# Kernel optimization log

Hardware: AMD Instinct MI355X
Metric: run time of the kernel (lower is better)

The kernel has to match this reference:

```python
import jax, jax.numpy as jnp
import numpy as np

B, C, N, F_, HID = 512, 3, 128, 256, 128  # batch, channels, nodes(=in_dim), num_f(=seq), gru hidden


def setup_inputs() -> dict:
    key = jax.random.key(0)
    ks = jax.random.split(key, 12)
    s = 0.05
    inp = {
        "X": jax.random.normal(ks[0], (B, N, F_), jnp.float32),
        "H": jax.random.uniform(ks[1], (B, C, N, N), jnp.float32),
        "weight": jnp.full((1, 1), 10.0, jnp.float32),        # nn.init.constant_(weight, 10)
        "soft": jnp.full((C,), 1.0 / C, jnp.float32),          # nn.init.constant_(soft, 1/C)
        "w_ih_f": jax.random.normal(ks[2], (3 * HID, N), jnp.float32) * s,
        "w_hh_f": jax.random.normal(ks[3], (3 * HID, HID), jnp.float32) * s,
        "b_ih_f": jax.random.normal(ks[4], (3 * HID,), jnp.float32) * s,
        "b_hh_f": jax.random.normal(ks[5], (3 * HID,), jnp.float32) * s,
        "w_ih_b": jax.random.normal(ks[6], (3 * HID, N), jnp.float32) * s,
        "w_hh_b": jax.random.normal(ks[7], (3 * HID, HID), jnp.float32) * s,
        "b_ih_b": jax.random.normal(ks[8], (3 * HID,), jnp.float32) * s,
        "b_hh_b": jax.random.normal(ks[9], (3 * HID,), jnp.float32) * s,
        "bn_gamma": jnp.ones((F_,), jnp.float32),
        "bn_beta": jnp.zeros((F_,), jnp.float32),
    }
    return inp


def _gru_dir(xs, w_ih, w_hh, b_ih, b_hh):
    # xs: [T, B, in] -> ys: [T, B, HID]; torch GRU cell equations
    def cell(h, x):
        gi = x @ w_ih.T + b_ih
        gh = h @ w_hh.T + b_hh
        i_r, i_z, i_n = jnp.split(gi, 3, axis=-1)
        h_r, h_z, h_n = jnp.split(gh, 3, axis=-1)
        r = jax.nn.sigmoid(i_r + h_r)
        z = jax.nn.sigmoid(i_z + h_z)
        n = jnp.tanh(i_n + r * h_n)
        h_new = (1.0 - z) * n + z * h
        return h_new, h_new
    h0 = jnp.zeros((xs.shape[1], w_hh.shape[1]), xs.dtype)
    _, ys = jax.lax.scan(cell, h0, xs)
    return ys


def reference(X, H, weight, soft, w_ih_f, w_hh_f, b_ih_f, b_hh_f,
              w_ih_b, w_hh_b, b_ih_b, b_hh_b, bn_gamma, bn_beta):
    n = X.shape[1]
    I = jnp.eye(n, dtype=X.dtype)
    # norm(): zero the diagonal, add identity, symmetric D^-1/2 H D^-1/2 (all C channels at once)
    Hn = H * (1.0 - I) + I                              # [B,C,N,N]
    deg = jnp.sum(Hn, axis=-1)                          # [B,C,N]
    dinv = deg ** -0.5
    Hn = dinv[..., :, None] * Hn * dinv[..., None, :]
    # gcn_conv across all features/channels in one einsum; weight is a 1x1 scalar
    HX = jnp.einsum('bcnm,bmf->bcnf', Hn, X) * weight[0, 0]
    Xc = jnp.sum(jax.nn.leaky_relu(HX, 0.01) * soft[None, :, None, None], axis=1)  # [B,N,F]
    # per1 -> [B, F, N]; GRU batch_first with seq_len=F, input=N
    xs = Xc.transpose(2, 0, 1)                          # [T=F, B, N]
    yf = _gru_dir(xs, w_ih_f, w_hh_f, b_ih_f, b_hh_f)
    yb = _gru_dir(xs[::-1], w_ih_b, w_hh_b, b_ih_b, b_hh_b)[::-1]
    y = jnp.concatenate([yf, yb], axis=-1).transpose(1, 0, 2)  # [B, F, 2*HID]

    # BatchNorm1d(num_f), training-mode batch stats over (batch, length) per channel F
    mean = jnp.mean(y, axis=(0, 2), keepdims=True)
    var = jnp.var(y, axis=(0, 2), keepdims=True)
    y = bn_gamma[None, :, None] * (y - mean) / jnp.sqrt(var + 1e-5) + bn_beta[None, :, None]
    # per2 -> [B, 2*HID, F]
    return y.transpose(0, 2, 1)
```

## Files before the change

kernel.cpp:

```cpp
#include <hip/hip_runtime.h>

typedef short s8v  __attribute__((ext_vector_type(8)));
typedef float f4v  __attribute__((ext_vector_type(4)));

#define B_   512
#define C_   3
#define N_   128
#define F_   256
#define T_   256
#define HID_ 128
#define G3_  384

__device__ __forceinline__ ushort f2bf(float f) {
  union { float f; unsigned u; } v; v.f = f;
  return (ushort)((v.u + 0x7FFFu + ((v.u >> 16) & 1u)) >> 16);
}
__device__ __forceinline__ float bf2f(ushort h) {
  union { unsigned u; float f; } v; v.u = ((unsigned)h) << 16;
  return v.f;
}
__device__ __forceinline__ float rcp_(float x) { return __builtin_amdgcn_rcpf(x); }
__device__ __forceinline__ float sigm(float x) { return rcp_(1.0f + __expf(-x)); }
__device__ __forceinline__ float tanh_(float x) { return 2.0f * rcp_(1.0f + __expf(-2.0f * x)) - 1.0f; }

#define LDS_BARRIER() asm volatile("s_waitcnt lgkmcnt(0)\n\ts_barrier" ::: "memory")

__global__ void k_wcvt(const float* __restrict__ a, const float* __restrict__ b,
                       const float* __restrict__ c, const float* __restrict__ d,
                       ushort* __restrict__ o) {
  int i = blockIdx.x * 256 + threadIdx.x;
  const float* src = (i < 49152) ? a : (i < 98304) ? b : (i < 147456) ? c : d;
  o[i] = f2bf(src[i % 49152]);
}

__global__ void k_dinv(const float* __restrict__ H, float* __restrict__ dinv) {
  const int bc = blockIdx.x;
  const int lane = threadIdx.x & 63, w = threadIdx.x >> 6;
  const float* Hm = H + (size_t)bc * N_ * N_;
  for (int r = w * 32; r < w * 32 + 32; ++r) {
    float a = Hm[(size_t)r * N_ + lane];
    float b = Hm[(size_t)r * N_ + 64 + lane];
    if (lane == r) a = 1.0f;
    if (64 + lane == r) b = 1.0f;
    float s = a + b;
    #pragma unroll
    for (int o = 32; o; o >>= 1) s += __shfl_xor(s, o);
    if (lane == 0) dinv[bc * N_ + r] = 1.0f / sqrtf(s);
  }
}

__global__ __launch_bounds__(256, 1) void k_conv(
    const float* __restrict__ X, const float* __restrict__ H,
    const float* __restrict__ dinv, const float* __restrict__ wscal,
    const float* __restrict__ soft, ushort* __restrict__ XcT) {
  __shared__ ushort hn[C_][N_][136];
  __shared__ ushort xt[N_][136];
  __shared__ float dv[C_ * N_];
  const int b = blockIdx.x;
  const int tid = threadIdx.x;
  const int lane = tid & 63, w = tid >> 6;
  const int rq = lane >> 4, l15 = lane & 15;

  for (int i = tid; i < C_ * N_; i += 256) dv[i] = dinv[b * C_ * N_ + i];
  __syncthreads();

  {
    const int m4 = (tid & 31) * 4;
    const int nof = tid >> 5;
    for (int c = 0; c < C_; ++c) {
      const float* Hm = H + ((size_t)(b * C_ + c)) * N_ * N_;
      const float* dvc = dv + c * N_;
      #pragma unroll
      for (int p = 0; p < 16; ++p) {
        int n = p * 8 + nof;
        float4 v = *(const float4*)&Hm[(size_t)n * N_ + m4];
        float f0 = (m4 + 0 == n) ? 1.0f : v.x;
        float f1 = (m4 + 1 == n) ? 1.0f : v.y;
        float f2 = (m4 + 2 == n) ? 1.0f : v.z;
        float f3 = (m4 + 3 == n) ? 1.0f : v.w;
        ushort4 o;
        o.x = f2bf(f0 * dvc[m4 + 0]);
        o.y = f2bf(f1 * dvc[m4 + 1]);
        o.z = f2bf(f2 * dvc[m4 + 2]);
        o.w = f2bf(f3 * dvc[m4 + 3]);
        *(ushort4*)&hn[c][n][m4] = o;
      }
    }
  }

  const float wmul = wscal[0];
  const float scf[3] = {soft[0], soft[1], soft[2]};

  for (int fh = 0; fh < 2; ++fh) {
    __syncthreads();
    {
      const int fl4 = (tid & 31) * 4;
      const int mof = tid >> 5;
      #pragma unroll
      for (int p = 0; p < 16; ++p) {
        int m = p * 8 + mof;
        float4 v = *(const float4*)&X[((size_t)b * N_ + m) * F_ + fh * 128 + fl4];
        xt[fl4 + 0][m] = f2bf(v.x);
        xt[fl4 + 1][m] = f2bf(v.y);
        xt[fl4 + 2][m] = f2bf(v.z);
        xt[fl4 + 3][m] = f2bf(v.w);
      }
    }
    __syncthreads();

    s8v af[2][4];
    #pragma unroll
    for (int rt = 0; rt < 2; ++rt)
      #pragma unroll
      for (int kk = 0; kk < 4; ++kk)
        af[rt][kk] = *(const s8v*)&xt[w * 32 + rt * 16 + l15][kk * 32 + rq * 8];

    f4v xc[2][8];
    #pragma unroll
    for (int rt = 0; rt < 2; ++rt)
      #pragma unroll
      for (int nt = 0; nt < 8; ++nt)
        xc[rt][nt] = (f4v){0.f, 0.f, 0.f, 0.f};

    for (int c = 0; c < C_; ++c) {
      f4v hx[2][8];
      #pragma unroll
      for (int rt = 0; rt < 2; ++rt)
        #pragma unroll
        for (int nt = 0; nt < 8; ++nt)
          hx[rt][nt] = (f4v){0.f, 0.f, 0.f, 0.f};
      #pragma unroll
      for (int kk = 0; kk < 4; ++kk) {
        #pragma unroll
        for (int nt = 0; nt < 8; ++nt) {
          s8v bf = *(const s8v*)&hn[c][nt * 16 + l15][kk * 32 + rq * 8];
          hx[0][nt] = __builtin_amdgcn_mfma_f32_16x16x32_bf16(af[0][kk], bf, hx[0][nt], 0, 0, 0);
          hx[1][nt] = __builtin_amdgcn_mfma_f32_16x16x32_bf16(af[1][kk], bf, hx[1][nt], 0, 0, 0);
        }
      }
      const float* dvc = dv + c * N_;
      const float s = scf[c];
      #pragma unroll
      for (int nt = 0; nt < 8; ++nt) {
        float dn = dvc[nt * 16 + l15] * wmul;
        #pragma unroll
        for (int i = 0; i < 4; ++i) {
          float v0 = hx[0][nt][i] * dn;
          xc[0][nt][i] += s * fmaxf(v0, 0.01f * v0);
          float v1 = hx[1][nt][i] * dn;
          xc[1][nt][i] += s * fmaxf(v1, 0.01f * v1);
        }
      }
    }
    __syncthreads();
    #pragma unroll
    for (int rt = 0; rt < 2; ++rt)
      #pragma unroll
      for (int nt = 0; nt < 8; ++nt)
        #pragma unroll
        for (int i = 0; i < 4; ++i)
          xt[w * 32 + rt * 16 + rq * 4 + i][nt * 16 + l15] = f2bf(xc[rt][nt][i]);
    __syncthreads();
    #pragma unroll
    for (int p = 0; p < 4; ++p) {
      int tl = p * 32 + (tid >> 3);
      int n0 = (tid & 7) * 16;
      size_t rowb = ((size_t)b * F_ + fh * 128 + tl) * N_;
      *(s8v*)&XcT[rowb + n0]     = *(const s8v*)&xt[tl][n0];
      *(s8v*)&XcT[rowb + n0 + 8] = *(const s8v*)&xt[tl][n0 + 8];
    }
  }
}

__global__ __launch_bounds__(512, 2) void k_gru(
    const ushort* __restrict__ XcT, const ushort* __restrict__ wbf,
    const float* __restrict__ bihf, const float* __restrict__ bhhf,
    const float* __restrict__ bihb, const float* __restrict__ bhhb,
    ushort* __restrict__ y) {
  __shared__ ushort hlds[2][16][136];
  __shared__ ushort xbuf[2][16][136];
  const int dir = blockIdx.x >> 5;
  const int chunk = blockIdx.x & 31;
  const int tid = threadIdx.x;
  const int lane = tid & 63, w = tid >> 6;
  const int rq = lane >> 4, l15 = lane & 15;
  const int jb = w * 16;
  const int jr = jb + rq * 4;
  const ushort* wih = wbf + (size_t)(dir * 2) * G3_ * HID_;
  const ushort* whh = wih + G3_ * HID_;
  const float* bih = dir ? bihb : bihf;
  const float* bhh = dir ? bhhb : bhhf;

  s8v fir[4], fiz[4], fin[4], fhr[4], fhz[4], fhn[4];
  #pragma unroll
  for (int kk = 0; kk < 4; ++kk) {
    const int ko = kk * 32 + rq * 8;
    const int row = jb + l15;
    fir[kk] = *(const s8v*)&wih[(size_t)(row)       * HID_ + ko];
    fiz[kk] = *(const s8v*)&wih[(size_t)(128 + row) * HID_ + ko];
    fin[kk] = *(const s8v*)&wih[(size_t)(256 + row) * HID_ + ko];
    fhr[kk] = *(const s8v*)&whh[(size_t)(row)       * HID_ + ko];
    fhz[kk] = *(const s8v*)&whh[(size_t)(128 + row) * HID_ + ko];
    fhn[kk] = *(const s8v*)&whh[(size_t)(256 + row) * HID_ + ko];
  }
  float4 bi_r = *(const float4*)&bih[jr],        bh_r = *(const float4*)&bhh[jr];
  float4 bi_z = *(const float4*)&bih[128 + jr],  bh_z = *(const float4*)&bhh[128 + jr];
  float4 bin4 = *(const float4*)&bih[256 + jr];
  float4 bhn4 = *(const float4*)&bhh[256 + jr];
  f4v br = {bi_r.x + bh_r.x, bi_r.y + bh_r.y, bi_r.z + bh_r.z, bi_r.w + bh_r.w};
  f4v bz = {bi_z.x + bh_z.x, bi_z.y + bh_z.y, bi_z.z + bh_z.z, bi_z.w + bh_z.w};
  f4v bin = {bin4.x, bin4.y, bin4.z, bin4.w};
  f4v bhn = {bhn4.x, bhn4.y, bhn4.z, bhn4.w};

  for (int i = tid; i < 16 * 136; i += 512) ((ushort*)hlds[0])[i] = 0;

  const int rr = tid >> 5;
  const int nq = (tid & 31) * 4;
  const size_t xrow = (size_t)(chunk * 16 + rr) * T_;
  {
    int t0 = dir ? (T_ - 1) : 0;
    *(ushort4*)&xbuf[0][rr][nq] = *(const ushort4*)&XcT[(xrow + t0) * N_ + nq];
  }
  f4v hreg = {0.f, 0.f, 0.f, 0.f};
  __syncthreads();

  for (int s = 0; s < T_; ++s) {
    const int cur = s & 1;
    const int t_in = dir ? (T_ - 1 - s) : s;
    const int sn = (s + 1 < T_) ? s + 1 : s;
    const int t_nx = dir ? (T_ - 1 - sn) : sn;
    ushort4 xn = *(const ushort4*)&XcT[(xrow + t_nx) * N_ + nq];

    f4v ar = br, az = bz, ain = bin, ahn = bhn;
    #pragma unroll
    for (int kk = 0; kk < 4; ++kk) {
      const int ko = kk * 32 + rq * 8;
      s8v xf = *(const s8v*)&xbuf[cur][l15][ko];
      s8v hf = *(const s8v*)&hlds[cur][l15][ko];
      ar  = __builtin_amdgcn_mfma_f32_16x16x32_bf16(fir[kk], xf, ar, 0, 0, 0);
      ar  = __builtin_amdgcn_mfma_f32_16x16x32_bf16(fhr[kk], hf, ar, 0, 0, 0);
      az  = __builtin_amdgcn_mfma_f32_16x16x32_bf16(fiz[kk], xf, az, 0, 0, 0);
      az  = __builtin_amdgcn_mfma_f32_16x16x32_bf16(fhz[kk], hf, az, 0, 0, 0);
      ain = __builtin_amdgcn_mfma_f32_16x16x32_bf16(fin[kk], xf, ain, 0, 0, 0);
      ahn = __builtin_amdgcn_mfma_f32_16x16x32_bf16(fhn[kk], hf, ahn, 0, 0, 0);
    }
    ushort hb[4];
    #pragma unroll
    for (int i = 0; i < 4; ++i) {
      float r = sigm(ar[i]);
      float z = sigm(az[i]);
      float n = tanh_(ain[i] + r * ahn[i]);
      float h = n + z * (hreg[i] - n);
      hreg[i] = h;
      hb[i] = f2bf(h);
    }
    ushort4 hv; hv.x = hb[0]; hv.y = hb[1]; hv.z = hb[2]; hv.w = hb[3];
    *(ushort4*)&y[((size_t)t_in * B_ + chunk * 16 + l15) * 256 + dir * 128 + jr] = hv;
    *(ushort4*)&hlds[cur ^ 1][l15][jr] = hv;
    *(ushort4*)&xbuf[cur ^ 1][rr][nq] = xn;
    LDS_BARRIER();
  }
}

__global__ void k_stats(const ushort* __restrict__ y, const float* __restrict__ gamma,
                        const float* __restrict__ beta, float* __restrict__ stats) {
  const int t = blockIdx.x, tid = threadIdx.x;
  const ushort* p = y + (size_t)t * 256 * B_;
  float s = 0.f, q = 0.f;
  for (int i = tid * 8; i < 256 * B_; i += 256 * 8) {
    s8v v = *(const s8v*)&p[i];
    #pragma unroll
    for (int e = 0; e < 8; ++e) {
      float f = bf2f((ushort)v[e]);
      s += f; q += f * f;
    }
  }
  #pragma unroll
  for (int o = 32; o; o >>= 1) { s += __shfl_xor(s, o); q += __shfl_xor(q, o); }
  __shared__ float rs[4], rq2[4];
  if ((tid & 63) == 0) { rs[tid >> 6] = s; rq2[tid >> 6] = q; }
  __syncthreads();
  if (tid == 0) {
    s = rs[0] + rs[1] + rs[2] + rs[3];
    q = rq2[0] + rq2[1] + rq2[2] + rq2[3];
    const float inv = 1.0f / (256.f * 512.f);
    float mean = s * inv;
    float var = q * inv - mean * mean;
    float istd = 1.0f / sqrtf(var + 1e-5f);
    float a = gamma[t] * istd;
    stats[2 * t] = a;
    stats[2 * t + 1] = beta[t] - mean * a;
  }
}

__global__ __launch_bounds__(256) void k_apply(
    const ushort* __restrict__ y, const float* __restrict__ stats,
    float* __restrict__ out) {
  __shared__ ushort tile[256][64];
  __shared__ float sA[256], sB[256];
  const int b = blockIdx.x;
  const int j0 = blockIdx.y * 64;
  const int tid = threadIdx.x;
  sA[tid] = stats[2 * tid];
  sB[tid] = stats[2 * tid + 1];
  {
    const ushort* src = &y[((size_t)tid * B_ + b) * 256 + j0];
    const int sw = (tid >> 5) & 7;
    #pragma unroll
    for (int q = 0; q < 8; ++q)
      *(s8v*)&tile[tid][(q ^ sw) * 8] = *(const s8v*)&src[q * 8];
  }
  __syncthreads();
  const int j = tid >> 2, jc = j >> 3, jrr = j & 7;
  const int tq = tid & 3;
  float* op = out + ((size_t)b * 256 + j0 + j) * 256 + tq * 64;
  #pragma unroll
  for (int k = 0; k < 16; ++k) {
    const int t = tq * 64 + k * 4;
    float4 o;
    #pragma unroll
    for (int e = 0; e < 4; ++e) {
      const int te = t + e;
      const int sw2 = (te >> 5) & 7;
      const int jcol = ((jc ^ sw2) * 8) + jrr;
      float vv = bf2f(tile[te][jcol]) * sA[te] + sB[te];
      if (e == 0) o.x = vv; else if (e == 1) o.y = vv; else if (e == 2) o.z = vv; else o.w = vv;
    }
    *(float4*)&op[k * 4] = o;
  }
}

extern "C" void kernel_launch(void* const* d_in, const int* in_sizes, int n_in,
                              void* d_out, int out_size, void* d_ws, size_t ws_size,
                              hipStream_t stream) {
  const float* X      = (const float*)d_in[0];
  const float* H      = (const float*)d_in[1];
  const float* weight = (const float*)d_in[2];
  const float* soft   = (const float*)d_in[3];
  const float* w_ih_f = (const float*)d_in[4];
  const float* w_hh_f = (const float*)d_in[5];
  const float* b_ih_f = (const float*)d_in[6];
  const float* b_hh_f = (const float*)d_in[7];
  const float* w_ih_b = (const float*)d_in[8];
  const float* w_hh_b = (const float*)d_in[9];
  const float* b_ih_b = (const float*)d_in[10];
  const float* b_hh_b = (const float*)d_in[11];
  const float* gamma  = (const float*)d_in[12];
  const float* beta   = (const float*)d_in[13];
  float* out = (float*)d_out;

  char* ws = (char*)d_ws;
  ushort* wbf   = (ushort*)(ws);
  float*  dinv  = (float*) (ws + 393216);
  ushort* XcT   = (ushort*)(ws + 1179648);
  ushort* ybuf  = (ushort*)(ws + 34734080);
  float*  stats = (float*) (ws + 101842944);

  k_wcvt<<<768, 256, 0, stream>>>(w_ih_f, w_hh_f, w_ih_b, w_hh_b, wbf);
  k_dinv<<<B_ * C_, 256, 0, stream>>>(H, dinv);
  k_conv<<<B_, 256, 0, stream>>>(X, H, dinv, weight, soft, XcT);
  k_gru<<<64, 512, 0, stream>>>(XcT, wbf, b_ih_f, b_hh_f, b_ih_b, b_hh_b, ybuf);
  k_stats<<<T_, 256, 0, stream>>>(ybuf, gamma, beta, stats);
  k_apply<<<dim3(512, 4), 256, 0, stream>>>(ybuf, stats, out);
}
```

Measured before the change: 403.4 us.

## Precompute normalized bf16 adjacency in separate kernel and shrink conv LDS for occupancy

Replaces the degree-only kernel with one that reads each H matrix once, computes row sums, and writes the fully normalized adjacency (both D^-1/2 factors) as bf16 to workspace. The conv kernel then streams each channel's bf16 matrix into a single LDS buffer instead of holding all three channels as fp32-derived tiles. This cuts the conv kernel's LDS footprint so two blocks can fit per CU, and it no longer re-reads fp32 H. The cost is an extra bf16 round trip through global memory (about 50 MB written and read back) and extra barriers per channel in the conv loop.

```diff
diff --git a/kernel.cpp b/kernel.cpp
--- a/kernel.cpp
+++ b/kernel.cpp
@@ -33,63 +33,58 @@
   o[i] = f2bf(src[i % 49152]);
 }
 
-__global__ void k_dinv(const float* __restrict__ H, float* __restrict__ dinv) {
+__global__ __launch_bounds__(256) void k_hnorm(const float* __restrict__ H,
+                                               ushort* __restrict__ Hn) {
+  __shared__ float dvr[N_];
   const int bc = blockIdx.x;
-  const int lane = threadIdx.x & 63, w = threadIdx.x >> 6;
-  const float* Hm = H + (size_t)bc * N_ * N_;
-  for (int r = w * 32; r < w * 32 + 32; ++r) {
-    float a = Hm[(size_t)r * N_ + lane];
-    float b = Hm[(size_t)r * N_ + 64 + lane];
-    if (lane == r) a = 1.0f;
-    if (64 + lane == r) b = 1.0f;
-    float s = a + b;
-    #pragma unroll
-    for (int o = 32; o; o >>= 1) s += __shfl_xor(s, o);
-    if (lane == 0) dinv[bc * N_ + r] = 1.0f / sqrtf(s);
-  }
-}
-
-__global__ __launch_bounds__(256, 1) void k_conv(
-    const float* __restrict__ X, const float* __restrict__ H,
-    const float* __restrict__ dinv, const float* __restrict__ wscal,
-    const float* __restrict__ soft, ushort* __restrict__ XcT) {
-  __shared__ ushort hn[C_][N_][136];
+  const int tid = threadIdx.x;
+  const int r = tid >> 1;
+  const int half = (tid & 1) * 64;
+  const float* src = H + (size_t)bc * N_ * N_ + (size_t)r * N_ + half;
+
+  float v[64];
+  #pragma unroll
+  for (int i = 0; i < 16; ++i) {
+    float4 q = *(const float4*)&src[i * 4];
+    v[i * 4 + 0] = q.x; v[i * 4 + 1] = q.y; v[i * 4 + 2] = q.z; v[i * 4 + 3] = q.w;
+  }
+  if ((r >> 6) == (tid & 1)) v[r & 63] = 1.0f;
+  float s = 0.f;
+  #pragma unroll
+  for (int i = 0; i < 64; ++i) s += v[i];
+  s += __shfl_xor(s, 1);
+  if ((tid & 1) == 0) dvr[r] = 1.0f / sqrtf(s);
+  __syncthreads();
+
+  const float dr = dvr[r];
+  ushort* dst = Hn + (size_t)bc * N_ * N_ + (size_t)r * N_ + half;
+  #pragma unroll
+  for (int i4 = 0; i4 < 16; ++i4) {
+    float4 dc = *(const float4*)&dvr[half + i4 * 4];
+    ushort4 o;
+    o.x = f2bf(v[i4 * 4 + 0] * dr * dc.x);
+    o.y = f2bf(v[i4 * 4 + 1] * dr * dc.y);
+    o.z = f2bf(v[i4 * 4 + 2] * dr * dc.z);
+    o.w = f2bf(v[i4 * 4 + 3] * dr * dc.w);
+    *(ushort4*)&dst[i4 * 4] = o;
+  }
+}
+
+__global__ __launch_bounds__(256, 2) void k_conv2(
+    const float* __restrict__ X, const ushort* __restrict__ Hn,
+    const float* __restrict__ wscal, const float* __restrict__ soft,
+    ushort* __restrict__ XcT) {
+  __shared__ ushort hc[N_][136];
   __shared__ ushort xt[N_][136];
-  __shared__ float dv[C_ * N_];
   const int b = blockIdx.x;
   const int tid = threadIdx.x;
   const int lane = tid & 63, w = tid >> 6;
   const int rq = lane >> 4, l15 = lane & 15;
-
-  for (int i = tid; i < C_ * N_; i += 256) dv[i] = dinv[b * C_ * N_ + i];
-  __syncthreads();
-
-  {
-    const int m4 = (tid & 31) * 4;
-    const int nof = tid >> 5;
-    for (int c = 0; c < C_; ++c) {
-      const float* Hm = H + ((size_t)(b * C_ + c)) * N_ * N_;
-      const float* dvc = dv + c * N_;
-      #pragma unroll
-      for (int p = 0; p < 16; ++p) {
-        int n = p * 8 + nof;
-        float4 v = *(const float4*)&Hm[(size_t)n * N_ + m4];
-        float f0 = (m4 + 0 == n) ? 1.0f : v.x;
-        float f1 = (m4 + 1 == n) ? 1.0f : v.y;
-        float f2 = (m4 + 2 == n) ? 1.0f : v.z;
-        float f3 = (m4 + 3 == n) ? 1.0f : v.w;
-        ushort4 o;
-        o.x = f2bf(f0 * dvc[m4 + 0]);
-        o.y = f2bf(f1 * dvc[m4 + 1]);
-        o.z = f2bf(f2 * dvc[m4 + 2]);
-        o.w = f2bf(f3 * dvc[m4 + 3]);
-        *(ushort4*)&hn[c][n][m4] = o;
-      }
-    }
-  }
-
   const float wmul = wscal[0];
   const float scf[3] = {soft[0], soft[1], soft[2]};
+  const ushort* Hb = Hn + (size_t)b * C_ * N_ * N_;
+  const int srow = tid >> 1;
+  const int scol = (tid & 1) * 64;
 
   for (int fh = 0; fh < 2; ++fh) {
     __syncthreads();
@@ -123,6 +118,15 @@
         xc[rt][nt] = (f4v){0.f, 0.f, 0.f, 0.f};
 
     for (int c = 0; c < C_; ++c) {
+      __syncthreads();
+      {
+        const ushort* hsrc = &Hb[((size_t)c * N_ + srow) * N_ + scol];
+        #pragma unroll
+        for (int p = 0; p < 8; ++p)
+          *(s8v*)&hc[srow][scol + p * 8] = *(const s8v*)&hsrc[p * 8];
+      }
+      __syncthreads();
+
       f4v hx[2][8];
       #pragma unroll
       for (int rt = 0; rt < 2; ++rt)
@@ -133,21 +137,19 @@
       for (int kk = 0; kk < 4; ++kk) {
         #pragma unroll
         for (int nt = 0; nt < 8; ++nt) {
-          s8v bf = *(const s8v*)&hn[c][nt * 16 + l15][kk * 32 + rq * 8];
+          s8v bf = *(const s8v*)&hc[nt * 16 + l15][kk * 32 + rq * 8];
           hx[0][nt] = __builtin_amdgcn_mfma_f32_16x16x32_bf16(af[0][kk], bf, hx[0][nt], 0, 0, 0);
           hx[1][nt] = __builtin_amdgcn_mfma_f32_16x16x32_bf16(af[1][kk], bf, hx[1][nt], 0, 0, 0);
         }
       }
-      const float* dvc = dv + c * N_;
       const float s = scf[c];
       #pragma unroll
       for (int nt = 0; nt < 8; ++nt) {
-        float dn = dvc[nt * 16 + l15] * wmul;
         #pragma unroll
         for (int i = 0; i < 4; ++i) {
-          float v0 = hx[0][nt][i] * dn;
+          float v0 = hx[0][nt][i] * wmul;
           xc[0][nt][i] += s * fmaxf(v0, 0.01f * v0);
-          float v1 = hx[1][nt][i] * dn;
+          float v1 = hx[1][nt][i] * wmul;
           xc[1][nt][i] += s * fmaxf(v1, 0.01f * v1);
         }
       }
@@ -351,14 +353,14 @@
 
   char* ws = (char*)d_ws;
   ushort* wbf   = (ushort*)(ws);
-  float*  dinv  = (float*) (ws + 393216);
-  ushort* XcT   = (ushort*)(ws + 1179648);
-  ushort* ybuf  = (ushort*)(ws + 34734080);
-  float*  stats = (float*) (ws + 101842944);
+  ushort* Hnb   = (ushort*)(ws + 393216);
+  ushort* XcT   = (ushort*)(ws + 50724864);
+  ushort* ybuf  = (ushort*)(ws + 84279296);
+  float*  stats = (float*) (ws + 151388160);
 
   k_wcvt<<<768, 256, 0, stream>>>(w_ih_f, w_hh_f, w_ih_b, w_hh_b, wbf);
-  k_dinv<<<B_ * C_, 256, 0, stream>>>(H, dinv);
-  k_conv<<<B_, 256, 0, stream>>>(X, H, dinv, weight, soft, XcT);
+  k_hnorm<<<B_ * C_, 256, 0, stream>>>(H, Hnb);
+  k_conv2<<<B_, 256, 0, stream>>>(X, Hnb, weight, soft, XcT);
   k_gru<<<64, 512, 0, stream>>>(XcT, wbf, b_ih_f, b_hh_f, b_ih_b, b_hh_b, ybuf);
   k_stats<<<T_, 256, 0, stream>>>(ybuf, gamma, beta, stats);
   k_apply<<<dim3(512, 4), 256, 0, stream>>>(ybuf, stats, out);
```

Measured after the change: 441.6 us. 9.5% more time.
